# Optimization experiments

Measured on AMD Instinct MI355X. Metric: run time of the kernel, lower is better.

The kernel has to match this reference:

```python
import jax, jax.numpy as jnp
import numpy as np

DROP_SCALE = 1e-4  # tf.multiply(feat_dropout, 0.0001)


def setup_inputs() -> dict:
    key = jax.random.key(0)
    k1, k2 = jax.random.split(key)
    B, C, N, D = 128, 2, 256, 256
    x = jax.random.normal(k1, (B, C, N, D), dtype=jnp.float32)
    # glorot_uniform for kernel [C*N*D, N]
    fan_in, fan_out = C * N * D, N
    limit = np.sqrt(6.0 / (fan_in + fan_out)).astype(np.float32)
    W = jax.random.uniform(k2, (fan_in, fan_out), dtype=jnp.float32,
                           minval=-limit, maxval=limit)
    return {"x": x, "W": W}


def _forward(x, W):
    B, C, N, D = x.shape
    K = N // 2  # with continuous data, exactly half strictly exceed the median
    # Keras Flatten(channels_first): permute to channels-last order, then flatten
    xf = jnp.transpose(x, (0, 2, 3, 1)).reshape(B, -1)          # [B, N*D*C]
    line = jax.nn.sigmoid(xf @ W)                                # [B, N]
    med = jnp.median(line, axis=-1, keepdims=True)               # [B, 1]
    mask = med < line                                            # [B, N] bool
    mask3 = jnp.broadcast_to(mask[:, None, :], (B, C, N))        # tile over channels
    # ragged boolean_mask + to_tensor == stable compaction of kept rows.
    # Stable argsort of (~mask) puts True (kept) positions first, in order.
    idx_att = jnp.argsort(~mask3, axis=-1, stable=True)[..., :K]   # [B, C, K]
    idx_drp = jnp.argsort(mask3, axis=-1, stable=True)[..., :K]    # [B, C, K]
    feat_att = jnp.take_along_axis(x, idx_att[..., None], axis=2)  # [B, C, K, D]
    feat_drp = jnp.take_along_axis(x, idx_drp[..., None], axis=2)  # [B, C, K, D]
    return feat_att + DROP_SCALE * feat_drp


def reference(x, W):
    return _forward(x, W)
```

## Files before the change

kernel.cpp:

```cpp
#include <hip/hip_runtime.h>
#include <hip/hip_bf16.h>

#define BATCH 128
#define CH    2
#define NN    256
#define DD    256
#define KTOT  131072
#define KHALF 128

#define KS    32
#define NTB   128
#define PITCH 40

typedef short bf16x8 __attribute__((ext_vector_type(8)));
typedef float f32x4  __attribute__((ext_vector_type(4)));

__device__ __forceinline__ void hilo2(float a, float b, unsigned& hp, unsigned& lp) {
    union { __hip_bfloat162 v; unsigned u; } H, L;
    H.v = __float22bfloat162_rn(float2{a, b});
    hp = H.u;
    float2 hf = __bfloat1622float2(H.v);
    L.v = __float22bfloat162_rn(float2{a - hf.x, b - hf.y});
    lp = L.u;
}

template <int SLICES, bool ATOMIC>
__global__ __launch_bounds__(256, 2) void gemm_mfma(const float* __restrict__ x,
                                                    const float* __restrict__ W,
                                                    float* __restrict__ zout) {
    constexpr int KLEN = KTOT / SLICES;
    constexpr int NST  = KLEN / KS;
    constexpr int NBLK = SLICES * 2;

    __shared__ unsigned short Ah[128][PITCH], Al[128][PITCH];
    __shared__ unsigned short Bh[NTB][PITCH], Bl[NTB][PITCH];

    const int bid     = blockIdx.x;
    const int logical = (bid & 7) * (NBLK >> 3) + (bid >> 3);
    const int s       = logical >> 1;
    const int nh      = logical & 1;

    const int t  = threadIdx.x;
    const int k0 = s * KLEN;
    const int c  = k0 >> 16;
    const int nd_base = k0 & 65535;

    const int ra = t & 127;
    const int ha = t >> 7;
    const int cb = t & 127;
    const int hb = t >> 7;

    const float* xrow = &x[(size_t)ra * KTOT + k0 + 16 * ha];
    const float* wcol = &W[(size_t)(2 * (nd_base + 16 * hb) + c) * NN + nh * NTB + cb];

    auto loadr = [&](float* av, float* bv, int st) {
        const float* xp = xrow + st * KS;
        *(float4*)&av[0]  = *(const float4*)&xp[0];
        *(float4*)&av[4]  = *(const float4*)&xp[4];
        *(float4*)&av[8]  = *(const float4*)&xp[8];
        *(float4*)&av[12] = *(const float4*)&xp[12];
        const float* wp = wcol + (size_t)st * KS * 2 * NN;
#pragma unroll
        for (int i = 0; i < 16; ++i)
            bv[i] = wp[(size_t)i * 2 * NN];
    };

    auto writest = [&](const float* av, const float* bv) {
        uint4 H0, H1, L0, L1;
        hilo2(av[0],  av[1],  H0.x, L0.x); hilo2(av[2],  av[3],  H0.y, L0.y);
        hilo2(av[4],  av[5],  H0.z, L0.z); hilo2(av[6],  av[7],  H0.w, L0.w);
        hilo2(av[8],  av[9],  H1.x, L1.x); hilo2(av[10], av[11], H1.y, L1.y);
        hilo2(av[12], av[13], H1.z, L1.z); hilo2(av[14], av[15], H1.w, L1.w);
        *(uint4*)&Ah[ra][16 * ha]     = H0;
        *(uint4*)&Ah[ra][16 * ha + 8] = H1;
        *(uint4*)&Al[ra][16 * ha]     = L0;
        *(uint4*)&Al[ra][16 * ha + 8] = L1;
        hilo2(bv[0],  bv[1],  H0.x, L0.x); hilo2(bv[2],  bv[3],  H0.y, L0.y);
        hilo2(bv[4],  bv[5],  H0.z, L0.z); hilo2(bv[6],  bv[7],  H0.w, L0.w);
        hilo2(bv[8],  bv[9],  H1.x, L1.x); hilo2(bv[10], bv[11], H1.y, L1.y);
        hilo2(bv[12], bv[13], H1.z, L1.z); hilo2(bv[14], bv[15], H1.w, L1.w);
        *(uint4*)&Bh[cb][16 * hb]     = H0;
        *(uint4*)&Bh[cb][16 * hb + 8] = H1;
        *(uint4*)&Bl[cb][16 * hb]     = L0;
        *(uint4*)&Bl[cb][16 * hb + 8] = L1;
    };

    const int lane = t & 63;
    const int wid  = t >> 6;
    const int wm   = (wid >> 1) * 64;
    const int wn   = (wid & 1) * 64;
    const int lr   = lane & 15;
    const int kq   = (lane >> 4) * 8;

    f32x4 acc[4][4] = {};

    auto compute = [&]() {
        bf16x8 a_h[4], a_l[4];
#pragma unroll
        for (int mt = 0; mt < 4; ++mt) {
            a_h[mt] = *(const bf16x8*)&Ah[wm + mt * 16 + lr][kq];
            a_l[mt] = *(const bf16x8*)&Al[wm + mt * 16 + lr][kq];
        }
#pragma unroll
        for (int nt = 0; nt < 4; ++nt) {
            bf16x8 b_h = *(const bf16x8*)&Bh[wn + nt * 16 + lr][kq];
            bf16x8 b_l = *(const bf16x8*)&Bl[wn + nt * 16 + lr][kq];
#pragma unroll
            for (int mt = 0; mt < 4; ++mt) {
                acc[mt][nt] = __builtin_amdgcn_mfma_f32_16x16x32_bf16(a_h[mt], b_h, acc[mt][nt], 0, 0, 0);
                acc[mt][nt] = __builtin_amdgcn_mfma_f32_16x16x32_bf16(a_h[mt], b_l, acc[mt][nt], 0, 0, 0);
                acc[mt][nt] = __builtin_amdgcn_mfma_f32_16x16x32_bf16(a_l[mt], b_h, acc[mt][nt], 0, 0, 0);
            }
        }
    };

    float avA[16], bvA[16], avB[16], bvB[16];
    loadr(avA, bvA, 0);
#pragma unroll
    for (int st = 0; st < NST; st += 2) {
        if (st + 1 < NST) loadr(avB, bvB, st + 1);
        __syncthreads();
        writest(avA, bvA);
        __syncthreads();
        compute();
        if (st + 2 < NST) loadr(avA, bvA, st + 2);
        __syncthreads();
        writest(avB, bvB);
        __syncthreads();
        compute();
    }

#pragma unroll
    for (int mt = 0; mt < 4; ++mt)
#pragma unroll
        for (int nt = 0; nt < 4; ++nt)
#pragma unroll
            for (int r = 0; r < 4; ++r) {
                const int row = wm + mt * 16 + (lane >> 4) * 4 + r;
                const int col = nh * NTB + wn + nt * 16 + lr;
                if (ATOMIC) atomicAdd(&zout[row * NN + col], acc[mt][nt][r]);
                else zout[(size_t)s * (BATCH * NN) + row * NN + col] = acc[mt][nt][r];
            }
}

template <int SLICES>
__global__ __launch_bounds__(256) void reduce1(const float* __restrict__ part,
                                               float* __restrict__ part2) {
    constexpr int GROUPS = SLICES / 32;
    const int g = blockIdx.x % GROUPS;
    const int b = blockIdx.x / GROUPS;
    const int j = threadIdx.x;
    float v = 0.0f;
#pragma unroll
    for (int i = 0; i < 32; ++i)
        v += part[(size_t)(g * 32 + i) * (BATCH * NN) + b * NN + j];
    part2[(size_t)g * (BATCH * NN) + b * NN + j] = v;
}

__global__ __launch_bounds__(256) void select_kernel(const float* __restrict__ p2, int ngroups,
                                                     int* __restrict__ idx_att,
                                                     int* __restrict__ idx_drp) {
    __shared__ float zv[NN];
    __shared__ int   flags[NN];
    const int b = blockIdx.x;
    const int j = threadIdx.x;
    float v = 0.0f;
    for (int g = 0; g < ngroups; ++g)
        v += p2[(size_t)g * (BATCH * NN) + b * NN + j];
    zv[j] = v;
    __syncthreads();
    int rank = 0;
    for (int i = 0; i < NN; ++i) {
        const float u = zv[i];
        rank += (u < v) || (u == v && i < j);
    }
    const int kept = (rank >= KHALF) ? 1 : 0;
    flags[j] = kept;
    __syncthreads();
    int pos = 0;
    for (int i = 0; i < j; ++i) pos += flags[i];
    if (kept) idx_att[b * KHALF + pos]       = j;
    else      idx_drp[b * KHALF + (j - pos)] = j;
}

__global__ __launch_bounds__(256) void gather_kernel(const float* __restrict__ x,
                                                     const int* __restrict__ idx_att,
                                                     const int* __restrict__ idx_drp,
                                                     float* __restrict__ out) {
    const int row  = blockIdx.x * 4 + (threadIdx.x >> 6);
    const int lane = threadIdx.x & 63;
    const int k = row & 127;
    const int c = (row >> 7) & 1;
    const int b = row >> 8;
    const int ia = idx_att[b * KHALF + k];
    const int id = idx_drp[b * KHALF + k];
    const float4* pa = (const float4*)&x[((b * 2 + c) * NN + ia) * DD];
    const float4* pd = (const float4*)&x[((b * 2 + c) * NN + id) * DD];
    float4* po = (float4*)&out[(size_t)row * DD];
    const float4 a  = pa[lane];
    const float4 d4 = pd[lane];
    float4 o;
    o.x = a.x + 1e-4f * d4.x;
    o.y = a.y + 1e-4f * d4.y;
    o.z = a.z + 1e-4f * d4.z;
    o.w = a.w + 1e-4f * d4.w;
    po[lane] = o;
}

extern "C" void kernel_launch(void* const* d_in, const int* in_sizes, int n_in,
                              void* d_out, int out_size, void* d_ws, size_t ws_size,
                              hipStream_t stream) {
    const float* x = (const float*)d_in[0];
    const float* W = (const float*)d_in[1];
    float* out = (float*)d_out;

    const size_t zrow   = (size_t)BATCH * NN * sizeof(float);
    const size_t idxB   = (size_t)BATCH * KHALF * sizeof(int);
    const size_t pA     = 512 * zrow;
    const size_t p2A    = 16 * zrow;
    const size_t pB     = 256 * zrow;
    const size_t p2B    = 8 * zrow;

    if (ws_size >= pA + p2A + 2 * idxB) {
        float* part    = (float*)d_ws;
        float* part2   = (float*)((char*)d_ws + pA);
        int*   idx_att = (int*)((char*)d_ws + pA + p2A);
        int*   idx_drp = idx_att + BATCH * KHALF;
        gemm_mfma<512, false><<<1024, 256, 0, stream>>>(x, W, part);
        reduce1<512><<<16 * BATCH, 256, 0, stream>>>(part, part2);
        select_kernel<<<BATCH, 256, 0, stream>>>(part2, 16, idx_att, idx_drp);
        gather_kernel<<<BATCH * CH * KHALF / 4, 256, 0, stream>>>(x, idx_att, idx_drp, out);
    } else if (ws_size >= pB + p2B + 2 * idxB) {
        float* part    = (float*)d_ws;
        float* part2   = (float*)((char*)d_ws + pB);
        int*   idx_att = (int*)((char*)d_ws + pB + p2B);
        int*   idx_drp = idx_att + BATCH * KHALF;
        gemm_mfma<256, false><<<512, 256, 0, stream>>>(x, W, part);
        reduce1<256><<<8 * BATCH, 256, 0, stream>>>(part, part2);
        select_kernel<<<BATCH, 256, 0, stream>>>(part2, 8, idx_att, idx_drp);
        gather_kernel<<<BATCH * CH * KHALF / 4, 256, 0, stream>>>(x, idx_att, idx_drp, out);
    } else {
        float* z       = (float*)d_ws;
        int*   idx_att = (int*)((char*)d_ws + zrow);
        int*   idx_drp = idx_att + BATCH * KHALF;
        hipMemsetAsync(z, 0, zrow, stream);
        gemm_mfma<512, true><<<1024, 256, 0, stream>>>(x, W, z);
        select_kernel<<<BATCH, 256, 0, stream>>>(z, 1, idx_att, idx_drp);
        gather_kernel<<<BATCH * CH * KHALF / 4, 256, 0, stream>>>(x, idx_att, idx_drp, out);
    }
}
```

Baseline: 298.6 us.

## Fuse split-K reduction, median select and gather into one kernel; retune GEMM pipeline

The GEMM now always uses 256 K-slices (512 blocks) with occupancy hint 3 and a deeper register prefetch: the next stage is loaded right after the current stage is written to LDS, with the loop no longer unrolled. The separate reduce, select and gather kernels are merged into one 1024-thread kernel per (batch, channel). Each block sums all partial slices, ranks the values to find the median, compacts the indices in LDS, and gathers the output rows. This removes two kernel launches and the global round-trips for part2 and the index arrays. In exchange, the selection work is done twice (once per channel), and the 512-slice configuration with its extra parallelism is gone.

```diff
diff --git a/kernel.cpp b/kernel.cpp
--- a/kernel.cpp
+++ b/kernel.cpp
@@ -8,9 +8,12 @@
 #define KTOT  131072
 #define KHALF 128
 
-#define KS    32
-#define NTB   128
-#define PITCH 40
+#define KSPLIT 256
+#define KLEN   (KTOT / KSPLIT)
+#define KS     32
+#define NST    (KLEN / KS)
+#define NTB    128
+#define PITCH  40
 
 typedef short bf16x8 __attribute__((ext_vector_type(8)));
 typedef float f32x4  __attribute__((ext_vector_type(4)));
@@ -24,19 +27,15 @@
     lp = L.u;
 }
 
-template <int SLICES, bool ATOMIC>
-__global__ __launch_bounds__(256, 2) void gemm_mfma(const float* __restrict__ x,
+template <bool ATOMIC>
+__global__ __launch_bounds__(256, 3) void gemm_mfma(const float* __restrict__ x,
                                                     const float* __restrict__ W,
                                                     float* __restrict__ zout) {
-    constexpr int KLEN = KTOT / SLICES;
-    constexpr int NST  = KLEN / KS;
-    constexpr int NBLK = SLICES * 2;
-
     __shared__ unsigned short Ah[128][PITCH], Al[128][PITCH];
     __shared__ unsigned short Bh[NTB][PITCH], Bl[NTB][PITCH];
 
     const int bid     = blockIdx.x;
-    const int logical = (bid & 7) * (NBLK >> 3) + (bid >> 3);
+    const int logical = (bid & 7) * 64 + (bid >> 3);
     const int s       = logical >> 1;
     const int nh      = logical & 1;
 
@@ -53,7 +52,7 @@
     const float* xrow = &x[(size_t)ra * KTOT + k0 + 16 * ha];
     const float* wcol = &W[(size_t)(2 * (nd_base + 16 * hb) + c) * NN + nh * NTB + cb];
 
-    auto loadr = [&](float* av, float* bv, int st) {
+    auto loadr = [&](float (&av)[16], float (&bv)[16], int st) {
         const float* xp = xrow + st * KS;
         *(float4*)&av[0]  = *(const float4*)&xp[0];
         *(float4*)&av[4]  = *(const float4*)&xp[4];
@@ -65,7 +64,7 @@
             bv[i] = wp[(size_t)i * 2 * NN];
     };
 
-    auto writest = [&](const float* av, const float* bv) {
+    auto writest = [&](const float (&av)[16], const float (&bv)[16]) {
         uint4 H0, H1, L0, L1;
         hilo2(av[0],  av[1],  H0.x, L0.x); hilo2(av[2],  av[3],  H0.y, L0.y);
         hilo2(av[4],  av[5],  H0.z, L0.z); hilo2(av[6],  av[7],  H0.w, L0.w);
@@ -116,16 +115,17 @@
 
     float avA[16], bvA[16], avB[16], bvB[16];
     loadr(avA, bvA, 0);
-#pragma unroll
+    loadr(avB, bvB, 1);
+#pragma unroll 1
     for (int st = 0; st < NST; st += 2) {
-        if (st + 1 < NST) loadr(avB, bvB, st + 1);
         __syncthreads();
         writest(avA, bvA);
+        if (st + 2 < NST) loadr(avA, bvA, st + 2);
         __syncthreads();
         compute();
-        if (st + 2 < NST) loadr(avA, bvA, st + 2);
         __syncthreads();
         writest(avB, bvB);
+        if (st + 3 < NST) loadr(avB, bvB, st + 3);
         __syncthreads();
         compute();
     }
@@ -143,68 +143,66 @@
             }
 }
 
-template <int SLICES>
-__global__ __launch_bounds__(256) void reduce1(const float* __restrict__ part,
-                                               float* __restrict__ part2) {
-    constexpr int GROUPS = SLICES / 32;
-    const int g = blockIdx.x % GROUPS;
-    const int b = blockIdx.x / GROUPS;
-    const int j = threadIdx.x;
+__global__ __launch_bounds__(1024) void select_gather(const float* __restrict__ part,
+                                                      int nslices,
+                                                      const float* __restrict__ x,
+                                                      float* __restrict__ out) {
+    __shared__ float zp[4][NN];
+    __shared__ float zs[NN];
+    __shared__ int   flags[NN];
+    __shared__ int   att_l[KHALF], drp_l[KHALF];
+
+    const int b = blockIdx.x >> 1;
+    const int cch = blockIdx.x & 1;
+    const int t = threadIdx.x;
+    const int j = t & 255;
+    const int g = t >> 8;
+
     float v = 0.0f;
-#pragma unroll
-    for (int i = 0; i < 32; ++i)
-        v += part[(size_t)(g * 32 + i) * (BATCH * NN) + b * NN + j];
-    part2[(size_t)g * (BATCH * NN) + b * NN + j] = v;
-}
-
-__global__ __launch_bounds__(256) void select_kernel(const float* __restrict__ p2, int ngroups,
-                                                     int* __restrict__ idx_att,
-                                                     int* __restrict__ idx_drp) {
-    __shared__ float zv[NN];
-    __shared__ int   flags[NN];
-    const int b = blockIdx.x;
-    const int j = threadIdx.x;
-    float v = 0.0f;
-    for (int g = 0; g < ngroups; ++g)
-        v += p2[(size_t)g * (BATCH * NN) + b * NN + j];
-    zv[j] = v;
-    __syncthreads();
-    int rank = 0;
-    for (int i = 0; i < NN; ++i) {
-        const float u = zv[i];
-        rank += (u < v) || (u == v && i < j);
-    }
-    const int kept = (rank >= KHALF) ? 1 : 0;
-    flags[j] = kept;
-    __syncthreads();
-    int pos = 0;
-    for (int i = 0; i < j; ++i) pos += flags[i];
-    if (kept) idx_att[b * KHALF + pos]       = j;
-    else      idx_drp[b * KHALF + (j - pos)] = j;
-}
-
-__global__ __launch_bounds__(256) void gather_kernel(const float* __restrict__ x,
-                                                     const int* __restrict__ idx_att,
-                                                     const int* __restrict__ idx_drp,
-                                                     float* __restrict__ out) {
-    const int row  = blockIdx.x * 4 + (threadIdx.x >> 6);
-    const int lane = threadIdx.x & 63;
-    const int k = row & 127;
-    const int c = (row >> 7) & 1;
-    const int b = row >> 8;
-    const int ia = idx_att[b * KHALF + k];
-    const int id = idx_drp[b * KHALF + k];
-    const float4* pa = (const float4*)&x[((b * 2 + c) * NN + ia) * DD];
-    const float4* pd = (const float4*)&x[((b * 2 + c) * NN + id) * DD];
-    float4* po = (float4*)&out[(size_t)row * DD];
-    const float4 a  = pa[lane];
-    const float4 d4 = pd[lane];
-    float4 o;
-    o.x = a.x + 1e-4f * d4.x;
-    o.y = a.y + 1e-4f * d4.y;
-    o.z = a.z + 1e-4f * d4.z;
-    o.w = a.w + 1e-4f * d4.w;
-    po[lane] = o;
+    for (int s2 = g; s2 < nslices; s2 += 4)
+        v += part[(size_t)s2 * (BATCH * NN) + b * NN + j];
+    zp[g][j] = v;
+    __syncthreads();
+
+    if (t < NN) zs[j] = zp[0][j] + zp[1][j] + zp[2][j] + zp[3][j];
+    __syncthreads();
+
+    if (t < NN) {
+        const float z = zs[j];
+        int rank = 0;
+        for (int i = 0; i < NN; ++i) {
+            const float u = zs[i];
+            rank += (u < z) || (u == z && i < j);
+        }
+        flags[j] = (rank >= KHALF) ? 1 : 0;
+    }
+    __syncthreads();
+    if (t < NN) {
+        int pos = 0;
+        for (int i = 0; i < j; ++i) pos += flags[i];
+        if (flags[j]) att_l[pos]     = j;
+        else          drp_l[j - pos] = j;
+    }
+    __syncthreads();
+
+    const int w    = t >> 6;
+    const int lane = t & 63;
+    const float* xc = &x[(size_t)(b * 2 + cch) * NN * DD];
+    float* oc = &out[(size_t)(b * 2 + cch) * KHALF * DD];
+#pragma unroll
+    for (int i = 0; i < 8; ++i) {
+        const int k  = w + 16 * i;
+        const int ia = att_l[k];
+        const int id = drp_l[k];
+        const float4 a  = ((const float4*)&xc[(size_t)ia * DD])[lane];
+        const float4 d4 = ((const float4*)&xc[(size_t)id * DD])[lane];
+        float4 o;
+        o.x = a.x + 1e-4f * d4.x;
+        o.y = a.y + 1e-4f * d4.y;
+        o.z = a.z + 1e-4f * d4.z;
+        o.w = a.w + 1e-4f * d4.w;
+        ((float4*)&oc[(size_t)k * DD])[lane] = o;
+    }
 }
 
 extern "C" void kernel_launch(void* const* d_in, const int* in_sizes, int n_in,
@@ -214,38 +212,17 @@
     const float* W = (const float*)d_in[1];
     float* out = (float*)d_out;
 
-    const size_t zrow   = (size_t)BATCH * NN * sizeof(float);
-    const size_t idxB   = (size_t)BATCH * KHALF * sizeof(int);
-    const size_t pA     = 512 * zrow;
-    const size_t p2A    = 16 * zrow;
-    const size_t pB     = 256 * zrow;
-    const size_t p2B    = 8 * zrow;
-
-    if (ws_size >= pA + p2A + 2 * idxB) {
-        float* part    = (float*)d_ws;
-        float* part2   = (float*)((char*)d_ws + pA);
-        int*   idx_att = (int*)((char*)d_ws + pA + p2A);
-        int*   idx_drp = idx_att + BATCH * KHALF;
-        gemm_mfma<512, false><<<1024, 256, 0, stream>>>(x, W, part);
-        reduce1<512><<<16 * BATCH, 256, 0, stream>>>(part, part2);
-        select_kernel<<<BATCH, 256, 0, stream>>>(part2, 16, idx_att, idx_drp);
-        gather_kernel<<<BATCH * CH * KHALF / 4, 256, 0, stream>>>(x, idx_att, idx_drp, out);
-    } else if (ws_size >= pB + p2B + 2 * idxB) {
-        float* part    = (float*)d_ws;
-        float* part2   = (float*)((char*)d_ws + pB);
-        int*   idx_att = (int*)((char*)d_ws + pB + p2B);
-        int*   idx_drp = idx_att + BATCH * KHALF;
-        gemm_mfma<256, false><<<512, 256, 0, stream>>>(x, W, part);
-        reduce1<256><<<8 * BATCH, 256, 0, stream>>>(part, part2);
-        select_kernel<<<BATCH, 256, 0, stream>>>(part2, 8, idx_att, idx_drp);
-        gather_kernel<<<BATCH * CH * KHALF / 4, 256, 0, stream>>>(x, idx_att, idx_drp, out);
+    const size_t zrow = (size_t)BATCH * NN * sizeof(float);
+    const size_t pB   = (size_t)KSPLIT * zrow;
+
+    if (ws_size >= pB) {
+        float* part = (float*)d_ws;
+        gemm_mfma<false><<<2 * KSPLIT, 256, 0, stream>>>(x, W, part);
+        select_gather<<<BATCH * CH, 1024, 0, stream>>>(part, KSPLIT, x, out);
     } else {
-        float* z       = (float*)d_ws;
-        int*   idx_att = (int*)((char*)d_ws + zrow);
-        int*   idx_drp = idx_att + BATCH * KHALF;
+        float* z = (float*)d_ws;
         hipMemsetAsync(z, 0, zrow, stream);
-        gemm_mfma<512, true><<<1024, 256, 0, stream>>>(x, W, z);
-        select_kernel<<<BATCH, 256, 0, stream>>>(z, 1, idx_att, idx_drp);
-        gather_kernel<<<BATCH * CH * KHALF / 4, 256, 0, stream>>>(x, idx_att, idx_drp, out);
-    }
-}
+        gemm_mfma<true><<<2 * KSPLIT, 256, 0, stream>>>(x, W, z);
+        select_gather<<<BATCH * CH, 1024, 0, stream>>>(z, 1, x, out);
+    }
+}
```

Measured after the change: 1.173 ms. 3.93x slower.
